# Optimization experiments

Hardware: AMD Instinct MI355X
Metric: run time of the kernel (lower is better)

## Reference

```python
import jax, jax.numpy as jnp
import numpy as np

B, T = 64, 500000

def setup_inputs() -> dict:
    key = jax.random.key(0)
    k1, k2 = jax.random.split(key)
    input_attenuation = jax.random.normal(k1, (B, T), dtype=jnp.float32)
    input_wet_dry = jax.random.randint(k2, (B, T), 0, 2).astype(jnp.bool_)
    return {"input_attenuation": input_attenuation, "input_wet_dry": input_wet_dry}

def reference(input_attenuation, input_wet_dry):
    # baseline[i] = baseline[i-1] if wet[i] else attenuation[i]; baseline[0] = attenuation[0].
    # Equivalent to gathering attenuation at the most recent 'dry' index (index 0 forced dry).
    Bn, Tn = input_attenuation.shape
    t = jnp.arange(Tn, dtype=jnp.int32)
    dry = jnp.logical_not(input_wet_dry).at[:, 0].set(True)  # timestep 0 always uses attenuation[0]
    pos = jnp.where(dry, t[None, :], jnp.int32(-1))          # [B, T]
    idx = jax.lax.associative_scan(jnp.maximum, pos, axis=1)  # running max = last dry index
    return jnp.take_along_axis(input_attenuation, idx, axis=1)
```

## Files before the change

kernel.cpp:

```cpp
#include <hip/hip_runtime.h>


constexpr int BATCH  = 4;
constexpr int WCHUNK = 256;
constexpr int OBLK   = BATCH * WCHUNK;
constexpr int WSEG   = 8192;
constexpr int OUTER  = WSEG / OBLK;

typedef float f4v __attribute__((ext_vector_type(4)));

__global__ __launch_bounds__(256) void ffill_wave_kernel(
    const float* __restrict__ att,
    const int* __restrict__ wet,
    float* __restrict__ out,
    int T, int segsPerRow)
{
    const int lane = threadIdx.x & 63;
    const int wid  = threadIdx.x >> 6;
    const int s    = blockIdx.x * 4 + wid;
    if (s >= segsPerRow) return;
    const int r    = blockIdx.y;
    const long long rowBase = (long long)r * T;
    const int base = s * WSEG;

    float carry = 0.0f;
    int hi = base;
    while (hi > 0) {
        const int start = (hi >= 64) ? (hi - 64) : 0;
        const int idx   = start + lane;
        bool dry = false;
        if (idx < hi) dry = (wet[rowBase + idx] == 0) || (idx == 0);
        const unsigned long long m = __ballot(dry);
        if (m != 0ull) {
            carry = att[rowBase + start + (63 - __clzll(m))];
            break;
        }
        hi = start;
    }

    float4 aC[BATCH]; int4 wC[BATCH];
    const int e0 = base + lane * 4;
    #pragma unroll
    for (int k = 0; k < BATCH; ++k) {
        const int e = e0 + k * WCHUNK;
        if (e < T) {
            aC[k] = *reinterpret_cast<const float4*>(att + rowBase + e);
            wC[k] = *reinterpret_cast<const int4*>(wet + rowBase + e);
        } else {
            aC[k] = make_float4(0.f, 0.f, 0.f, 0.f);
            wC[k] = make_int4(1, 1, 1, 1);
        }
    }

    for (int ot = 0; ot < OUTER; ++ot) {
        float4 aN[BATCH]; int4 wN[BATCH];
        #pragma unroll
        for (int k = 0; k < BATCH; ++k) {
            aN[k] = make_float4(0.f, 0.f, 0.f, 0.f);
            wN[k] = make_int4(1, 1, 1, 1);
        }
        if (ot + 1 < OUTER) {
            const int eb = e0 + (ot + 1) * OBLK;
            #pragma unroll
            for (int k = 0; k < BATCH; ++k) {
                const int e = eb + k * WCHUNK;
                if (e < T) {
                    aN[k] = *reinterpret_cast<const float4*>(att + rowBase + e);
                    wN[k] = *reinterpret_cast<const int4*>(wet + rowBase + e);
                }
            }
        }

        #pragma unroll
        for (int k = 0; k < BATCH; ++k) {
            const int e = e0 + ot * OBLK + k * WCHUNK;
            const bool valid = (e < T);

            bool d0 = (wC[k].x == 0) || (e == 0);
            bool d1 = (wC[k].y == 0);
            bool d2 = (wC[k].z == 0);
            bool d3 = (wC[k].w == 0);
            if (!valid) { d0 = d1 = d2 = d3 = false; }

            const bool has = d0 | d1 | d2 | d3;
            const float lastval = d3 ? aC[k].w : (d2 ? aC[k].z : (d1 ? aC[k].y : aC[k].x));

            const unsigned long long mask = __ballot(has);
            const unsigned long long pm = mask & ((1ull << lane) - 1ull);
            const int psrc = (pm != 0ull) ? (63 - __clzll(pm)) : 0;
            const float pval = __shfl(lastval, psrc);
            const float carry_in = (pm != 0ull) ? pval : carry;

            float running = carry_in;
            f4v o;
            running = d0 ? aC[k].x : running;  o.x = running;
            running = d1 ? aC[k].y : running;  o.y = running;
            running = d2 ? aC[k].z : running;  o.z = running;
            running = d3 ? aC[k].w : running;  o.w = running;
            if (valid) {
                __builtin_nontemporal_store(o, reinterpret_cast<f4v*>(out + rowBase + e));
            }

            carry = __shfl(running, 63);
        }

        #pragma unroll
        for (int k = 0; k < BATCH; ++k) { aC[k] = aN[k]; wC[k] = wN[k]; }
    }
}

extern "C" void kernel_launch(void* const* d_in, const int* in_sizes, int n_in,
                              void* d_out, int out_size, void* d_ws, size_t ws_size,
                              hipStream_t stream) {
    const float* att = (const float*)d_in[0];
    const int* wet   = (const int*)d_in[1];
    float* out       = (float*)d_out;

    const int B = 64;
    const int T = in_sizes[0] / B;
    const int segsPerRow = (T + WSEG - 1) / WSEG;
    const int blocksX = (segsPerRow + 3) / 4;

    dim3 grid(blocksX, B);
    dim3 block(256);
    ffill_wave_kernel<<<grid, block, 0, stream>>>(att, wet, out, T, segsPerRow);
}
```

Measured before the change: 312.7 us.

## Shrink wave segments to 2048 and overlap lookback with chunk-local scans

Each wave now handles a 2048-element segment held entirely in registers instead of 8192 elements streamed through a double buffer. That raises the number of waves and the memory parallelism. All loads, including a 64-element lookback window, are issued up front. Per-chunk ballot/shuffle scans are computed before the carry is known, so the serial carry chain becomes a simple select chain. The backward search for the last dry element is now paid by four times as many segments, and register pressure rises from holding eight chunks at once.

```diff
diff --git a/kernel.cpp b/kernel.cpp
--- a/kernel.cpp
+++ b/kernel.cpp
@@ -1,15 +1,13 @@
 #include <hip/hip_runtime.h>
 
 
-constexpr int BATCH  = 4;
+constexpr int K      = 8;
 constexpr int WCHUNK = 256;
-constexpr int OBLK   = BATCH * WCHUNK;
-constexpr int WSEG   = 8192;
-constexpr int OUTER  = WSEG / OBLK;
+constexpr int WSEG   = K * WCHUNK;
 
 typedef float f4v __attribute__((ext_vector_type(4)));
 
-__global__ __launch_bounds__(256) void ffill_wave_kernel(
+__global__ __launch_bounds__(256) void ffill_kernel(
     const float* __restrict__ att,
     const int* __restrict__ wet,
     float* __restrict__ out,
@@ -23,89 +21,93 @@
     const long long rowBase = (long long)r * T;
     const int base = s * WSEG;
 
-    float carry = 0.0f;
-    int hi = base;
-    while (hi > 0) {
-        const int start = (hi >= 64) ? (hi - 64) : 0;
-        const int idx   = start + lane;
-        bool dry = false;
-        if (idx < hi) dry = (wet[rowBase + idx] == 0) || (idx == 0);
-        const unsigned long long m = __ballot(dry);
-        if (m != 0ull) {
-            carry = att[rowBase + start + (63 - __clzll(m))];
-            break;
-        }
-        hi = start;
+    float att_lb = 0.0f; int wet_lb = 1;
+    if (base > 0) {
+        const int idx = base - 64 + lane;
+        att_lb = att[rowBase + idx];
+        wet_lb = wet[rowBase + idx];
     }
 
-    float4 aC[BATCH]; int4 wC[BATCH];
     const int e0 = base + lane * 4;
+    float4 a[K]; int4 w[K];
     #pragma unroll
-    for (int k = 0; k < BATCH; ++k) {
+    for (int k = 0; k < K; ++k) {
         const int e = e0 + k * WCHUNK;
         if (e < T) {
-            aC[k] = *reinterpret_cast<const float4*>(att + rowBase + e);
-            wC[k] = *reinterpret_cast<const int4*>(wet + rowBase + e);
+            a[k] = *reinterpret_cast<const float4*>(att + rowBase + e);
+            w[k] = *reinterpret_cast<const int4*>(wet + rowBase + e);
         } else {
-            aC[k] = make_float4(0.f, 0.f, 0.f, 0.f);
-            wC[k] = make_int4(1, 1, 1, 1);
+            a[k] = make_float4(0.f, 0.f, 0.f, 0.f);
+            w[k] = make_int4(1, 1, 1, 1);
         }
     }
 
-    for (int ot = 0; ot < OUTER; ++ot) {
-        float4 aN[BATCH]; int4 wN[BATCH];
-        #pragma unroll
-        for (int k = 0; k < BATCH; ++k) {
-            aN[k] = make_float4(0.f, 0.f, 0.f, 0.f);
-            wN[k] = make_int4(1, 1, 1, 1);
-        }
-        if (ot + 1 < OUTER) {
-            const int eb = e0 + (ot + 1) * OBLK;
-            #pragma unroll
-            for (int k = 0; k < BATCH; ++k) {
-                const int e = eb + k * WCHUNK;
-                if (e < T) {
-                    aN[k] = *reinterpret_cast<const float4*>(att + rowBase + e);
-                    wN[k] = *reinterpret_cast<const int4*>(wet + rowBase + e);
+    bool  d0v[K], d1v[K], d2v[K], d3v[K];
+    bool  anyDry[K];
+    float lastDry[K];
+    float preVal[K];  bool preHas[K];
+    #pragma unroll
+    for (int k = 0; k < K; ++k) {
+        const int e = e0 + k * WCHUNK;
+        const bool valid = (e < T);
+        bool d0 = (w[k].x == 0) || (e == 0);
+        bool d1 = (w[k].y == 0);
+        bool d2 = (w[k].z == 0);
+        bool d3 = (w[k].w == 0);
+        if (!valid) { d0 = d1 = d2 = d3 = false; }
+        d0v[k] = d0; d1v[k] = d1; d2v[k] = d2; d3v[k] = d3;
+
+        const bool has = d0 | d1 | d2 | d3;
+        const float lastval = d3 ? a[k].w : (d2 ? a[k].z : (d1 ? a[k].y : a[k].x));
+
+        const unsigned long long mask = __ballot(has);
+        anyDry[k] = (mask != 0ull);
+        const int wsrc = anyDry[k] ? (63 - __clzll(mask)) : 0;
+        lastDry[k] = __shfl(lastval, wsrc);
+
+        const unsigned long long pm = mask & ((1ull << lane) - 1ull);
+        preHas[k] = (pm != 0ull);
+        const int psrc = preHas[k] ? (63 - __clzll(pm)) : 0;
+        preVal[k] = __shfl(lastval, psrc);
+    }
+
+    float carry = 0.0f;
+    if (base > 0) {
+        const unsigned long long m = __ballot(wet_lb == 0);
+        if (m != 0ull) {
+            carry = __shfl(att_lb, 63 - __clzll(m));
+        } else {
+            int hi = base - 64;
+            while (hi > 0) {
+                const int start = (hi >= 64) ? (hi - 64) : 0;
+                const int idx   = start + lane;
+                const bool dry  = (idx < hi) && ((wet[rowBase + idx] == 0) || (idx == 0));
+                const unsigned long long mm = __ballot(dry);
+                if (mm != 0ull) {
+                    carry = att[rowBase + start + (63 - __clzll(mm))];
+                    break;
                 }
+                hi = start;
             }
         }
+    }
 
-        #pragma unroll
-        for (int k = 0; k < BATCH; ++k) {
-            const int e = e0 + ot * OBLK + k * WCHUNK;
-            const bool valid = (e < T);
+    #pragma unroll
+    for (int k = 0; k < K; ++k) {
+        const int e = e0 + k * WCHUNK;
+        const float carry_in = preHas[k] ? preVal[k] : carry;
 
-            bool d0 = (wC[k].x == 0) || (e == 0);
-            bool d1 = (wC[k].y == 0);
-            bool d2 = (wC[k].z == 0);
-            bool d3 = (wC[k].w == 0);
-            if (!valid) { d0 = d1 = d2 = d3 = false; }
-
-            const bool has = d0 | d1 | d2 | d3;
-            const float lastval = d3 ? aC[k].w : (d2 ? aC[k].z : (d1 ? aC[k].y : aC[k].x));
-
-            const unsigned long long mask = __ballot(has);
-            const unsigned long long pm = mask & ((1ull << lane) - 1ull);
-            const int psrc = (pm != 0ull) ? (63 - __clzll(pm)) : 0;
-            const float pval = __shfl(lastval, psrc);
-            const float carry_in = (pm != 0ull) ? pval : carry;
-
-            float running = carry_in;
-            f4v o;
-            running = d0 ? aC[k].x : running;  o.x = running;
-            running = d1 ? aC[k].y : running;  o.y = running;
-            running = d2 ? aC[k].z : running;  o.z = running;
-            running = d3 ? aC[k].w : running;  o.w = running;
-            if (valid) {
-                __builtin_nontemporal_store(o, reinterpret_cast<f4v*>(out + rowBase + e));
-            }
-
-            carry = __shfl(running, 63);
+        float running = carry_in;
+        f4v o;
+        running = d0v[k] ? a[k].x : running;  o.x = running;
+        running = d1v[k] ? a[k].y : running;  o.y = running;
+        running = d2v[k] ? a[k].z : running;  o.z = running;
+        running = d3v[k] ? a[k].w : running;  o.w = running;
+        if (e < T) {
+            __builtin_nontemporal_store(o, reinterpret_cast<f4v*>(out + rowBase + e));
         }
 
-        #pragma unroll
-        for (int k = 0; k < BATCH; ++k) { aC[k] = aN[k]; wC[k] = wN[k]; }
+        carry = anyDry[k] ? lastDry[k] : carry;
     }
 }
 
@@ -123,5 +125,5 @@
 
     dim3 grid(blocksX, B);
     dim3 block(256);
-    ffill_wave_kernel<<<grid, block, 0, stream>>>(att, wet, out, T, segsPerRow);
+    ffill_kernel<<<grid, block, 0, stream>>>(att, wet, out, T, segsPerRow);
 }
```

New measurement: 314.2 us. Within noise of the previous version (+0.5%).
